# Optimization experiments

Measured on AMD Instinct MI355X. Metric: run time of the kernel, lower is better.

## Reference

```python
import jax, jax.numpy as jnp
import numpy as np

B, H, W, C = 4, 64, 64, 256
DQK = C // 16  # query/key channels = 16


def setup_inputs() -> dict:
    key = jax.random.key(0)
    ks = jax.random.split(key, 8)
    s = 0.05
    return {
        "x": jax.random.normal(ks[0], (B, H, W, C), dtype=jnp.float32),
        "wq": jax.random.normal(ks[1], (C, DQK), dtype=jnp.float32) * s,
        "bq": jax.random.normal(ks[2], (DQK,), dtype=jnp.float32) * s,
        "wk": jax.random.normal(ks[3], (C, DQK), dtype=jnp.float32) * s,
        "bk": jax.random.normal(ks[4], (DQK,), dtype=jnp.float32) * s,
        "wv": jax.random.normal(ks[5], (C, C), dtype=jnp.float32) * s,
        "bv": jax.random.normal(ks[6], (C,), dtype=jnp.float32) * s,
        "gamma": jax.random.normal(ks[7], (), dtype=jnp.float32),
    }


def reference(x, wq, bq, wk, bk, wv, bv, gamma):
    # 1x1 convs == per-pixel linear projections
    q = jnp.einsum('bhwc,cd->bhwd', x, wq) + bq          # [B,H,W,DQK]
    k = jnp.einsum('bhwc,cd->bhwd', x, wk) + bk          # [B,H,W,DQK]
    v = jnp.einsum('bhwc,cd->bhwd', x, wv) + bv          # [B,H,W,C]
    hw = H * W
    q = q.reshape(B, hw, DQK)
    k = k.reshape(B, hw, DQK)
    v = v.reshape(B, hw, C)
    energy = jnp.einsum('bnd,bmd->bnm', q, k)            # [B,HW,HW]
    attention = jax.nn.softmax(energy, axis=-1)
    out = jnp.einsum('bnm,bmc->bnc', attention, v)       # [B,HW,C]
    out = out.reshape(B, H, W, C)
    return out * gamma + x, attention
```

## Files before the change

### kernel.cpp

```cpp
#include <hip/hip_runtime.h>

typedef _Float16 half8 __attribute__((ext_vector_type(8)));
typedef _Float16 half4v __attribute__((ext_vector_type(4)));
typedef __fp16 fp16x2 __attribute__((ext_vector_type(2)));
typedef float f32x16 __attribute__((ext_vector_type(16)));
typedef float f32x4 __attribute__((ext_vector_type(4)));
typedef unsigned int uint2v __attribute__((ext_vector_type(2)));
typedef unsigned int uint4v __attribute__((ext_vector_type(4)));

#define MFMA16(a, b, c) __builtin_amdgcn_mfma_f32_32x32x16_f16((a), (b), (c), 0, 0, 0)
#define QSC 1.44269504088896f

#define OFF_WB   0
#define OFF_WQK  131072
#define OFF_QF   147456
#define OFF_KF   671744
#define OFF_VB   1196032
#define OFF_MLP  9584640

__device__ inline unsigned int pkf16(float a, float b) {
    union { fp16x2 h; unsigned int u; } cv;
    cv.h = __builtin_amdgcn_cvt_pkrtz(a, b);
    return cv.u;
}
__device__ inline half8 mk8(unsigned int w0, unsigned int w1, unsigned int w2, unsigned int w3) {
    union { unsigned int u[4]; half8 h; } cv;
    cv.u[0] = w0; cv.u[1] = w1; cv.u[2] = w2; cv.u[3] = w3; return cv.h;
}

__global__ __launch_bounds__(256) void k_prep(const float* __restrict__ wq,
                                              const float* __restrict__ wk,
                                              const float* __restrict__ wv,
                                              _Float16* __restrict__ WB,
                                              _Float16* __restrict__ WQK) {
    int idx = blockIdx.x * 256 + threadIdx.x;
    if (idx < 65536) {
        int j = idx & 7, l = (idx >> 3) & 63, kc = idx >> 12;
        int ct = (idx >> 9) & 7;
        int k = kc * 16 + (l >> 5) * 8 + j;
        int c = ct * 32 + (l & 31);
        WB[idx] = (_Float16)wv[k * 256 + c];
    } else if (idx < 65536 + 8192) {
        int t = idx - 65536;
        int j = t & 7, l = (t >> 3) & 63, kc = t >> 9;
        int k = kc * 16 + (l >> 5) * 8 + j;
        int c = l & 31;
        WQK[t] = (_Float16)((c < 16) ? wq[k * 16 + c] : wk[k * 16 + (c - 16)]);
    }
}

__global__ __launch_bounds__(256, 2) void k_proj(const float* __restrict__ x,
                                                 const float* __restrict__ bq,
                                                 const float* __restrict__ bk,
                                                 const float* __restrict__ bv,
                                                 const _Float16* __restrict__ WB,
                                                 const _Float16* __restrict__ WQK,
                                                 _Float16* __restrict__ Qf,
                                                 _Float16* __restrict__ Kf,
                                                 _Float16* __restrict__ VB) {
    const int tid = threadIdx.x;
    const int w = tid >> 6, l = tid & 63, lo = l & 31, h = l >> 5;
    const long rowbase = (long)blockIdx.x * 32;
    const float* xp = x + (rowbase + lo) * 256 + h * 8;

    f32x16 acc0 = {}, acc1 = {}, accQK = {};
#pragma unroll
    for (int kc = 0; kc < 16; ++kc) {
        float4 a0 = *(const float4*)(xp + kc * 16);
        float4 a1 = *(const float4*)(xp + kc * 16 + 4);
        half8 xf;
        xf[0] = (_Float16)a0.x; xf[1] = (_Float16)a0.y; xf[2] = (_Float16)a0.z; xf[3] = (_Float16)a0.w;
        xf[4] = (_Float16)a1.x; xf[5] = (_Float16)a1.y; xf[6] = (_Float16)a1.z; xf[7] = (_Float16)a1.w;
        half8 b0 = *(const half8*)(WB + ((kc * 8 + 2 * w) * 64 + l) * 8);
        half8 b1 = *(const half8*)(WB + ((kc * 8 + 2 * w + 1) * 64 + l) * 8);
        acc0 = MFMA16(xf, b0, acc0);
        acc1 = MFMA16(xf, b1, acc1);
        if (w == 0) {
            half8 bqk = *(const half8*)(WQK + (kc * 64 + l) * 8);
            accQK = MFMA16(xf, bqk, accQK);
        }
    }

    const int b = (int)(rowbase >> 12);
    const int k16base = (int)((rowbase & 4095) >> 4);
#pragma unroll
    for (int cti = 0; cti < 2; ++cti) {
        int ct = 2 * w + cti;
        f32x16 acc = cti ? acc1 : acc0;
        float bias = bv[ct * 32 + lo];
#pragma unroll
        for (int g = 0; g < 4; ++g) {
            int K16 = k16base + (g >> 1);
            int lanep = (g & 1) * 32 + lo;
            _Float16* dst = VB + ((((long)b * 256 + K16) * 8 + ct) * 64 + lanep) * 8 + 4 * h;
            half4v pv;
            pv[0] = (_Float16)(acc[4 * g + 0] + bias);
            pv[1] = (_Float16)(acc[4 * g + 1] + bias);
            pv[2] = (_Float16)(acc[4 * g + 2] + bias);
            pv[3] = (_Float16)(acc[4 * g + 3] + bias);
            *(half4v*)dst = pv;
        }
    }
    if (w == 0) {
        float bias = (lo < 16) ? bq[lo] : bk[lo - 16];
#pragma unroll
        for (int r = 0; r < 16; ++r) {
            int kl = (r & 3) + 8 * (r >> 2) + 4 * h;
            long n = rowbase + kl;
            float v = accQK[r] + bias;
            if (lo < 16) Qf[n * 16 + lo] = (_Float16)(v * QSC);
            else         Kf[n * 16 + (lo - 16)] = (_Float16)v;
        }
    }
}

__global__ __launch_bounds__(256, 4) void k_ml(const _Float16* __restrict__ Qf,
                                               const _Float16* __restrict__ Kf,
                                               float2* __restrict__ MLp) {
    const int bid = blockIdx.x;
    const int kh = bid & 1;
    const int qi = bid >> 1;
    const int b = qi >> 7, qt = qi & 127;
    const int tid = threadIdx.x, w = tid >> 6, l = tid & 63, lo = l & 31, h = l >> 5;
    const int qbase = qt * 32;

    half8 qf = *(const half8*)(Qf + (((long)b * 4096 + qbase + lo) << 4) + h * 8);
    const _Float16* Kb = Kf + ((long)b * 4096 << 4);

    float m = -3e38f, lsum = 0.f;
    for (int i = 0; i < 16; ++i) {
        int t = kh * 64 + i * 4 + w;
        half8 kf = *(const half8*)(Kb + ((t * 32 + lo) << 4) + h * 8);
        f32x16 e = MFMA16(kf, qf, (f32x16){});
        float t0 = fmaxf(fmaxf(e[0], e[1]), fmaxf(e[2], e[3]));
        float t1 = fmaxf(fmaxf(e[4], e[5]), fmaxf(e[6], e[7]));
        float t2 = fmaxf(fmaxf(e[8], e[9]), fmaxf(e[10], e[11]));
        float t3 = fmaxf(fmaxf(e[12], e[13]), fmaxf(e[14], e[15]));
        float tmax = fmaxf(fmaxf(t0, t1), fmaxf(t2, t3));
        tmax = fmaxf(tmax, __shfl_xor(tmax, 32));
        if (tmax > m) { lsum *= exp2f(m - tmax); m = tmax; }
        float ss = 0.f;
#pragma unroll
        for (int r = 0; r < 16; ++r) ss += exp2f(e[r] - m);
        lsum += ss;
    }
    lsum += __shfl_xor(lsum, 32);

    __shared__ float sm[4][32];
    __shared__ float sl[4][32];
    if (l < 32) { sm[w][lo] = m; sl[w][lo] = lsum; }
    __syncthreads();
    if (tid < 32) {
        float M = fmaxf(fmaxf(sm[0][tid], sm[1][tid]), fmaxf(sm[2][tid], sm[3][tid]));
        float L = sl[0][tid] * exp2f(sm[0][tid] - M) + sl[1][tid] * exp2f(sm[1][tid] - M) +
                  sl[2][tid] * exp2f(sm[2][tid] - M) + sl[3][tid] * exp2f(sm[3][tid] - M);
        float2 v; v.x = M; v.y = L;
        MLp[(((long)b * 4096 + qbase + tid) << 1) + kh] = v;
    }
}

#define RS 260
__global__ __launch_bounds__(256, 4) void k_attn(const float* __restrict__ x,
                                                 const float* __restrict__ gptr,
                                                 const _Float16* __restrict__ Qf,
                                                 const _Float16* __restrict__ Kf,
                                                 const _Float16* __restrict__ VB,
                                                 const float2* __restrict__ MLp,
                                                 float* __restrict__ out0,
                                                 float* __restrict__ attn) {
    const int bid = blockIdx.x;
    const int xcd = bid & 7, slot = bid >> 3;
    const int b = xcd >> 1;
    const int qt = (xcd & 1) * 64 + (slot & 63);
    const int sp = slot >> 6;
    const int tid = threadIdx.x, w = tid >> 6, l = tid & 63, lo = l & 31, h = l >> 5;
    const int qbase = qt * 32;

    half8 qf = *(const half8*)(Qf + (((long)b * 4096 + qbase + lo) << 4) + h * 8);
    const _Float16* Kb = Kf + ((long)b * 4096 << 4);

    const float2* mlrow = MLp + ((long)(b * 4096 + qbase + lo) << 1);
    float2 mla = mlrow[0];
    float2 mlc = mlrow[1];
    float Mrow = fmaxf(mla.x, mlc.x);
    const float S_lane = Mrow + __log2f(mla.y * exp2f(mla.x - Mrow) + mlc.y * exp2f(mlc.x - Mrow));

    const _Float16* vb = VB + (long)b * 256 * 8 * 64 * 8;

    __shared__ unsigned int pc[32 * RS];

    const int srow = tid >> 3;
    const int st7 = tid & 7;
    float* aout = attn + (long)b * 4096 * 4096 + ((long)(qbase + srow) << 12);

    f32x16 oacc[4] = {};

    for (int i = 0; i < 32; ++i) {
        int t = i * 4 + w;
        half8 kf = *(const half8*)(Kb + ((t * 32 + lo) << 4) + h * 8);
        f32x16 e = MFMA16(kf, qf, (f32x16){});
        float p[16];
#pragma unroll
        for (int r = 0; r < 16; ++r) p[r] = exp2f(e[r] - S_lane);

        unsigned int u0 = pkf16(p[0], p[1]),   x0 = pkf16(p[4], p[5]);
        unsigned int v0 = pkf16(p[2], p[3]),   y0 = pkf16(p[6], p[7]);
        unsigned int u1 = pkf16(p[8], p[9]),   x1 = pkf16(p[12], p[13]);
        unsigned int v1 = pkf16(p[10], p[11]), y1 = pkf16(p[14], p[15]);
        uint2v t0 = __builtin_amdgcn_permlane32_swap(u0, x0, false, false);
        uint2v t1 = __builtin_amdgcn_permlane32_swap(v0, y0, false, false);
        uint2v t2 = __builtin_amdgcn_permlane32_swap(u1, x1, false, false);
        uint2v t3 = __builtin_amdgcn_permlane32_swap(v1, y1, false, false);
        half8 pa0 = mk8(t0.x, t1.x, t0.y, t1.y);
        half8 pa1 = mk8(t2.x, t3.x, t2.y, t3.y);

        if ((i >> 4) == sp) {
            int base = lo * RS + ((i & 3) << 6) + (w << 4) + (h << 2);
            *(uint4v*)&pc[base]     = (uint4v){t0.x, t1.x, t0.y, t1.y};
            *(uint4v*)&pc[base + 8] = (uint4v){t2.x, t3.x, t2.y, t3.y};
            if ((i & 3) == 3) {
                __syncthreads();
                float* ap = aout + (i - 3) * 128 + st7 * 4;
                const unsigned int* src = &pc[srow * RS + st7 * 2];
#pragma unroll
                for (int seg = 0; seg < 16; ++seg) {
                    uint2v u = *(const uint2v*)(src + seg * 16);
                    union { unsigned int u; fp16x2 h; } a, c;
                    a.u = u.x; c.u = u.y;
                    f32x4 ov = { (float)a.h[0], (float)a.h[1], (float)c.h[0], (float)c.h[1] };
                    *(f32x4*)(ap + seg * 32) = ov;
                }
                __syncthreads();
            }
        }

#pragma unroll
        for (int ct = 0; ct < 4; ++ct) {
            int ctg = 4 * sp + ct;
            half8 vf0 = *(const half8*)(vb + (((long)(2 * t + 0) * 8 + ctg) * 64 + l) * 8);
            half8 vf1 = *(const half8*)(vb + (((long)(2 * t + 1) * 8 + ctg) * 64 + l) * 8);
            oacc[ct] = MFMA16(pa0, vf0, oacc[ct]);
            oacc[ct] = MFMA16(pa1, vf1, oacc[ct]);
        }
    }

    float* fO = (float*)pc;
#pragma unroll 1
    for (int ww = 0; ww < 4; ++ww) {
        __syncthreads();
        if (w == ww) {
#pragma unroll
            for (int ct = 0; ct < 4; ++ct) {
#pragma unroll
                for (int r = 0; r < 16; ++r) {
                    int row = (r & 3) + 8 * (r >> 2) + 4 * h;
                    float val = oacc[ct][r];
                    if (ww == 0) fO[row * 132 + ct * 32 + lo] = val;
                    else         fO[row * 132 + ct * 32 + lo] += val;
                }
            }
        }
    }
    __syncthreads();

    float gamma = *gptr;
    int cb = st7 << 4;
    long base = ((long)b * 4096 + qbase + srow) * 256 + sp * 128 + cb;
    const float* xp = x + base;
    float* op = out0 + base;
#pragma unroll
    for (int c0 = 0; c0 < 16; c0 += 4) {
        float4 xv = *(const float4*)(xp + c0);
        f32x4 ov;
        ov.x = gamma * fO[srow * 132 + cb + c0 + 0] + xv.x;
        ov.y = gamma * fO[srow * 132 + cb + c0 + 1] + xv.y;
        ov.z = gamma * fO[srow * 132 + cb + c0 + 2] + xv.z;
        ov.w = gamma * fO[srow * 132 + cb + c0 + 3] + xv.w;
        *(f32x4*)(op + c0) = ov;
    }
}

extern "C" void kernel_launch(void* const* d_in, const int* in_sizes, int n_in,
                              void* d_out, int out_size, void* d_ws, size_t ws_size,
                              hipStream_t stream) {
    const float* x  = (const float*)d_in[0];
    const float* wq = (const float*)d_in[1];
    const float* bq = (const float*)d_in[2];
    const float* wk = (const float*)d_in[3];
    const float* bk = (const float*)d_in[4];
    const float* wv = (const float*)d_in[5];
    const float* bv = (const float*)d_in[6];
    const float* gamma = (const float*)d_in[7];

    char* ws = (char*)d_ws;
    _Float16* WB  = (_Float16*)(ws + OFF_WB);
    _Float16* WQK = (_Float16*)(ws + OFF_WQK);
    _Float16* Qf  = (_Float16*)(ws + OFF_QF);
    _Float16* Kf  = (_Float16*)(ws + OFF_KF);
    _Float16* VB  = (_Float16*)(ws + OFF_VB);
    float2*   MLp = (float2*)(ws + OFF_MLP);

    float* out0 = (float*)d_out;
    float* attn = (float*)d_out + 4194304;

    k_prep<<<288, 256, 0, stream>>>(wq, wk, wv, WB, WQK);
    k_proj<<<512, 256, 0, stream>>>(x, bq, bk, bv, WB, WQK, Qf, Kf, VB);
    k_ml  <<<1024, 256, 0, stream>>>(Qf, Kf, MLp);
    k_attn<<<1024, 256, 0, stream>>>(x, gamma, Qf, Kf, VB, MLp, out0, attn);
}
```

Before: 152.4 us.

## Warp-specialize attention kernel: compute waves produce, store waves write attention map

Doubles the block to 512 threads. Four waves compute QK, exp and PV MFMAs, and four extra waves stream the fp16 probability tiles from a double-buffered shared staging area out to the fp32 attention matrix. The loop order is changed so each compute group of four tiles stashes its own half before the other, letting the stores of group g-1 overlap with the compute of group g. The cost is twice the shared memory, extra idle waves, and higher register pressure from launch_bounds(512,4), which may lower occupancy.

```diff
diff --git a/kernel.cpp b/kernel.cpp
--- a/kernel.cpp
+++ b/kernel.cpp
@@ -159,8 +159,8 @@
     }
 }
 
-#define RS 260
-__global__ __launch_bounds__(256, 4) void k_attn(const float* __restrict__ x,
+#define RSg 260
+__global__ __launch_bounds__(512, 4) void k_attn(const float* __restrict__ x,
                                                  const float* __restrict__ gptr,
                                                  const _Float16* __restrict__ Qf,
                                                  const _Float16* __restrict__ Kf,
@@ -173,82 +173,111 @@
     const int b = xcd >> 1;
     const int qt = (xcd & 1) * 64 + (slot & 63);
     const int sp = slot >> 6;
-    const int tid = threadIdx.x, w = tid >> 6, l = tid & 63, lo = l & 31, h = l >> 5;
+    const int tid = threadIdx.x;
+    const int wv8 = tid >> 6;
+    const bool isComp = wv8 < 4;
+    const int w = wv8 & 3;
+    const int l = tid & 63, lo = l & 31, h = l >> 5;
     const int qbase = qt * 32;
 
-    half8 qf = *(const half8*)(Qf + (((long)b * 4096 + qbase + lo) << 4) + h * 8);
+    __shared__ unsigned int pc[2][32 * RSg];
+
     const _Float16* Kb = Kf + ((long)b * 4096 << 4);
-
-    const float2* mlrow = MLp + ((long)(b * 4096 + qbase + lo) << 1);
-    float2 mla = mlrow[0];
-    float2 mlc = mlrow[1];
-    float Mrow = fmaxf(mla.x, mlc.x);
-    const float S_lane = Mrow + __log2f(mla.y * exp2f(mla.x - Mrow) + mlc.y * exp2f(mlc.x - Mrow));
-
     const _Float16* vb = VB + (long)b * 256 * 8 * 64 * 8;
 
-    __shared__ unsigned int pc[32 * RS];
-
-    const int srow = tid >> 3;
-    const int st7 = tid & 7;
-    float* aout = attn + (long)b * 4096 * 4096 + ((long)(qbase + srow) << 12);
+    half8 qf = {};
+    float S_lane = 0.f;
+    if (isComp) {
+        qf = *(const half8*)(Qf + (((long)b * 4096 + qbase + lo) << 4) + h * 8);
+        const float2* mlrow = MLp + ((long)(b * 4096 + qbase + lo) << 1);
+        float2 mla = mlrow[0];
+        float2 mlc = mlrow[1];
+        float Mrow = fmaxf(mla.x, mlc.x);
+        S_lane = Mrow + __log2f(mla.y * exp2f(mla.x - Mrow) + mlc.y * exp2f(mlc.x - Mrow));
+    }
+
+    const int stid = tid & 255;
+    const int srow = stid >> 3, st7 = stid & 7;
+    float* aoutrow = attn + (long)b * 4096 * 4096 + ((long)(qbase + srow) << 12) + sp * 2048;
 
     f32x16 oacc[4] = {};
 
-    for (int i = 0; i < 32; ++i) {
-        int t = i * 4 + w;
-        half8 kf = *(const half8*)(Kb + ((t * 32 + lo) << 4) + h * 8);
-        f32x16 e = MFMA16(kf, qf, (f32x16){});
-        float p[16];
-#pragma unroll
-        for (int r = 0; r < 16; ++r) p[r] = exp2f(e[r] - S_lane);
-
-        unsigned int u0 = pkf16(p[0], p[1]),   x0 = pkf16(p[4], p[5]);
-        unsigned int v0 = pkf16(p[2], p[3]),   y0 = pkf16(p[6], p[7]);
-        unsigned int u1 = pkf16(p[8], p[9]),   x1 = pkf16(p[12], p[13]);
-        unsigned int v1 = pkf16(p[10], p[11]), y1 = pkf16(p[14], p[15]);
-        uint2v t0 = __builtin_amdgcn_permlane32_swap(u0, x0, false, false);
-        uint2v t1 = __builtin_amdgcn_permlane32_swap(v0, y0, false, false);
-        uint2v t2 = __builtin_amdgcn_permlane32_swap(u1, x1, false, false);
-        uint2v t3 = __builtin_amdgcn_permlane32_swap(v1, y1, false, false);
-        half8 pa0 = mk8(t0.x, t1.x, t0.y, t1.y);
-        half8 pa1 = mk8(t2.x, t3.x, t2.y, t3.y);
-
-        if ((i >> 4) == sp) {
-            int base = lo * RS + ((i & 3) << 6) + (w << 4) + (h << 2);
-            *(uint4v*)&pc[base]     = (uint4v){t0.x, t1.x, t0.y, t1.y};
-            *(uint4v*)&pc[base + 8] = (uint4v){t2.x, t3.x, t2.y, t3.y};
-            if ((i & 3) == 3) {
-                __syncthreads();
-                float* ap = aout + (i - 3) * 128 + st7 * 4;
-                const unsigned int* src = &pc[srow * RS + st7 * 2];
-#pragma unroll
-                for (int seg = 0; seg < 16; ++seg) {
-                    uint2v u = *(const uint2v*)(src + seg * 16);
-                    union { unsigned int u; fp16x2 h; } a, c;
-                    a.u = u.x; c.u = u.y;
-                    f32x4 ov = { (float)a.h[0], (float)a.h[1], (float)c.h[0], (float)c.h[1] };
-                    *(f32x4*)(ap + seg * 32) = ov;
+#pragma unroll 1
+    for (int g = 0; g < 4; ++g) {
+        if (isComp) {
+#pragma unroll
+            for (int li = 0; li < 4; ++li) {
+#pragma unroll
+                for (int which = 0; which < 2; ++which) {
+                    const bool stash = (which == 0);
+                    const int i = (stash ? sp : (1 - sp)) * 16 + g * 4 + li;
+                    const int t = i * 4 + w;
+                    half8 kf = *(const half8*)(Kb + ((t * 32 + lo) << 4) + h * 8);
+                    f32x16 e = MFMA16(kf, qf, (f32x16){});
+                    float p[16];
+#pragma unroll
+                    for (int r = 0; r < 16; ++r) p[r] = exp2f(e[r] - S_lane);
+
+                    unsigned int u0 = pkf16(p[0], p[1]),   x0 = pkf16(p[4], p[5]);
+                    unsigned int v0 = pkf16(p[2], p[3]),   y0 = pkf16(p[6], p[7]);
+                    unsigned int u1 = pkf16(p[8], p[9]),   x1 = pkf16(p[12], p[13]);
+                    unsigned int v1 = pkf16(p[10], p[11]), y1 = pkf16(p[14], p[15]);
+                    uint2v t0 = __builtin_amdgcn_permlane32_swap(u0, x0, false, false);
+                    uint2v t1 = __builtin_amdgcn_permlane32_swap(v0, y0, false, false);
+                    uint2v t2 = __builtin_amdgcn_permlane32_swap(u1, x1, false, false);
+                    uint2v t3 = __builtin_amdgcn_permlane32_swap(v1, y1, false, false);
+                    half8 pa0 = mk8(t0.x, t1.x, t0.y, t1.y);
+                    half8 pa1 = mk8(t2.x, t3.x, t2.y, t3.y);
+
+                    if (stash) {
+                        int base = lo * RSg + (li << 6) + (w << 4) + (h << 2);
+                        *(uint4v*)&pc[g & 1][base]     = (uint4v){t0.x, t1.x, t0.y, t1.y};
+                        *(uint4v*)&pc[g & 1][base + 8] = (uint4v){t2.x, t3.x, t2.y, t3.y};
+                    }
+
+#pragma unroll
+                    for (int ct = 0; ct < 4; ++ct) {
+                        int ctg = 4 * sp + ct;
+                        half8 vf0 = *(const half8*)(vb + (((long)(2 * t + 0) * 8 + ctg) * 64 + l) * 8);
+                        half8 vf1 = *(const half8*)(vb + (((long)(2 * t + 1) * 8 + ctg) * 64 + l) * 8);
+                        oacc[ct] = MFMA16(pa0, vf0, oacc[ct]);
+                        oacc[ct] = MFMA16(pa1, vf1, oacc[ct]);
+                    }
                 }
-                __syncthreads();
             }
-        }
-
-#pragma unroll
-        for (int ct = 0; ct < 4; ++ct) {
-            int ctg = 4 * sp + ct;
-            half8 vf0 = *(const half8*)(vb + (((long)(2 * t + 0) * 8 + ctg) * 64 + l) * 8);
-            half8 vf1 = *(const half8*)(vb + (((long)(2 * t + 1) * 8 + ctg) * 64 + l) * 8);
-            oacc[ct] = MFMA16(pa0, vf0, oacc[ct]);
-            oacc[ct] = MFMA16(pa1, vf1, oacc[ct]);
-        }
-    }
-
-    float* fO = (float*)pc;
+        } else if (g > 0) {
+            const unsigned int* src = &pc[(g - 1) & 1][srow * RSg + st7 * 2];
+            float* ap = aoutrow + (g - 1) * 512 + st7 * 4;
+#pragma unroll
+            for (int seg = 0; seg < 16; ++seg) {
+                uint2v u = *(const uint2v*)(src + seg * 16);
+                union { unsigned int u; fp16x2 h; } ua, uc;
+                ua.u = u.x; uc.u = u.y;
+                f32x4 ov = { (float)ua.h[0], (float)ua.h[1], (float)uc.h[0], (float)uc.h[1] };
+                *(f32x4*)(ap + seg * 32) = ov;
+            }
+        }
+        __syncthreads();
+    }
+
+    if (!isComp) {
+        const unsigned int* src = &pc[1][srow * RSg + st7 * 2];
+        float* ap = aoutrow + 3 * 512 + st7 * 4;
+#pragma unroll
+        for (int seg = 0; seg < 16; ++seg) {
+            uint2v u = *(const uint2v*)(src + seg * 16);
+            union { unsigned int u; fp16x2 h; } ua, uc;
+            ua.u = u.x; uc.u = u.y;
+            f32x4 ov = { (float)ua.h[0], (float)ua.h[1], (float)uc.h[0], (float)uc.h[1] };
+            *(f32x4*)(ap + seg * 32) = ov;
+        }
+    }
+
+    float* fO = (float*)&pc[0][0];
 #pragma unroll 1
     for (int ww = 0; ww < 4; ++ww) {
         __syncthreads();
-        if (w == ww) {
+        if (isComp && w == ww) {
 #pragma unroll
             for (int ct = 0; ct < 4; ++ct) {
 #pragma unroll
@@ -263,20 +292,22 @@
     }
     __syncthreads();
 
-    float gamma = *gptr;
-    int cb = st7 << 4;
-    long base = ((long)b * 4096 + qbase + srow) * 256 + sp * 128 + cb;
-    const float* xp = x + base;
-    float* op = out0 + base;
-#pragma unroll
-    for (int c0 = 0; c0 < 16; c0 += 4) {
-        float4 xv = *(const float4*)(xp + c0);
-        f32x4 ov;
-        ov.x = gamma * fO[srow * 132 + cb + c0 + 0] + xv.x;
-        ov.y = gamma * fO[srow * 132 + cb + c0 + 1] + xv.y;
-        ov.z = gamma * fO[srow * 132 + cb + c0 + 2] + xv.z;
-        ov.w = gamma * fO[srow * 132 + cb + c0 + 3] + xv.w;
-        *(f32x4*)(op + c0) = ov;
+    if (!isComp) {
+        float gamma = *gptr;
+        int cb = st7 << 4;
+        long base = ((long)b * 4096 + qbase + srow) * 256 + sp * 128 + cb;
+        const float* xp = x + base;
+        float* op = out0 + base;
+#pragma unroll
+        for (int c0 = 0; c0 < 16; c0 += 4) {
+            float4 xv = *(const float4*)(xp + c0);
+            f32x4 ov;
+            ov.x = gamma * fO[srow * 132 + cb + c0 + 0] + xv.x;
+            ov.y = gamma * fO[srow * 132 + cb + c0 + 1] + xv.y;
+            ov.z = gamma * fO[srow * 132 + cb + c0 + 2] + xv.z;
+            ov.w = gamma * fO[srow * 132 + cb + c0 + 3] + xv.w;
+            *(f32x4*)(op + c0) = ov;
+        }
     }
 }
 
@@ -306,5 +337,5 @@
     k_prep<<<288, 256, 0, stream>>>(wq, wk, wv, WB, WQK);
     k_proj<<<512, 256, 0, stream>>>(x, bq, bk, bv, WB, WQK, Qf, Kf, VB);
     k_ml  <<<1024, 256, 0, stream>>>(Qf, Kf, MLp);
-    k_attn<<<1024, 256, 0, stream>>>(x, gamma, Qf, Kf, VB, MLp, out0, attn);
-}
+    k_attn<<<1024, 512, 0, stream>>>(x, gamma, Qf, Kf, VB, MLp, out0, attn);
+}
```

New measurement: 224.1 us. 47.0% more time.

## Stage fp16 attention probabilities in workspace and expand to fp32 in separate kernel

Applied to the files above, without the earlier changes.

The attention kernel no longer writes the fp32 attention matrix directly. It now stores fp16 probability tiles into a workspace buffer with simple contiguous stores. A new k_expand kernel then reads that buffer and writes the fp32 attention rows in full-row coalesced order. The aim is to take the large strided fp32 stores off the compute-heavy kernel, at the cost of an extra launch and an extra write plus read of about 128MB of fp16 data.

```diff
diff --git a/kernel.cpp b/kernel.cpp
--- a/kernel.cpp
+++ b/kernel.cpp
@@ -17,6 +17,7 @@
 #define OFF_KF   671744
 #define OFF_VB   1196032
 #define OFF_MLP  9584640
+#define OFF_PF   16777216
 
 __device__ inline unsigned int pkf16(float a, float b) {
     union { fp16x2 h; unsigned int u; } cv;
@@ -159,7 +160,7 @@
     }
 }
 
-#define RS 260
+#define RSg 260
 __global__ __launch_bounds__(256, 4) void k_attn(const float* __restrict__ x,
                                                  const float* __restrict__ gptr,
                                                  const _Float16* __restrict__ Qf,
@@ -167,7 +168,7 @@
                                                  const _Float16* __restrict__ VB,
                                                  const float2* __restrict__ MLp,
                                                  float* __restrict__ out0,
-                                                 float* __restrict__ attn) {
+                                                 unsigned int* __restrict__ Pf) {
     const int bid = blockIdx.x;
     const int xcd = bid & 7, slot = bid >> 3;
     const int b = xcd >> 1;
@@ -187,11 +188,9 @@
 
     const _Float16* vb = VB + (long)b * 256 * 8 * 64 * 8;
 
-    __shared__ unsigned int pc[32 * RS];
-
-    const int srow = tid >> 3;
-    const int st7 = tid & 7;
-    float* aout = attn + (long)b * 4096 * 4096 + ((long)(qbase + srow) << 12);
+    __shared__ unsigned int pc[32 * RSg];
+
+    unsigned int* PfT = Pf + (long)(b * 128 + qt) * 8 * 8192;
 
     f32x16 oacc[4] = {};
 
@@ -215,20 +214,18 @@
         half8 pa1 = mk8(t2.x, t3.x, t2.y, t3.y);
 
         if ((i >> 4) == sp) {
-            int base = lo * RS + ((i & 3) << 6) + (w << 4) + (h << 2);
+            int li = i & 3;
+            int base = lo * RSg + (li << 6) + (w << 4) + (h << 2);
             *(uint4v*)&pc[base]     = (uint4v){t0.x, t1.x, t0.y, t1.y};
             *(uint4v*)&pc[base + 8] = (uint4v){t2.x, t3.x, t2.y, t3.y};
-            if ((i & 3) == 3) {
+            if (li == 3) {
                 __syncthreads();
-                float* ap = aout + (i - 3) * 128 + st7 * 4;
-                const unsigned int* src = &pc[srow * RS + st7 * 2];
-#pragma unroll
-                for (int seg = 0; seg < 16; ++seg) {
-                    uint2v u = *(const uint2v*)(src + seg * 16);
-                    union { unsigned int u; fp16x2 h; } a, c;
-                    a.u = u.x; c.u = u.y;
-                    f32x4 ov = { (float)a.h[0], (float)a.h[1], (float)c.h[0], (float)c.h[1] };
-                    *(f32x4*)(ap + seg * 32) = ov;
+                int G = sp * 4 + ((i >> 2) & 3);
+                unsigned int* dst = PfT + (long)G * 8192;
+#pragma unroll
+                for (int it = 0; it < 8; ++it) {
+                    uint4v v = *(const uint4v*)&pc[(it * 4 + w) * RSg + l * 4];
+                    *(uint4v*)(dst + it * 1024 + w * 256 + l * 4) = v;
                 }
                 __syncthreads();
             }
@@ -264,6 +261,7 @@
     __syncthreads();
 
     float gamma = *gptr;
+    const int srow = tid >> 3, st7 = tid & 7;
     int cb = st7 << 4;
     long base = ((long)b * 4096 + qbase + srow) * 256 + sp * 128 + cb;
     const float* xp = x + base;
@@ -277,6 +275,33 @@
         ov.z = gamma * fO[srow * 132 + cb + c0 + 2] + xv.z;
         ov.w = gamma * fO[srow * 132 + cb + c0 + 3] + xv.w;
         *(f32x4*)(op + c0) = ov;
+    }
+}
+
+__global__ __launch_bounds__(256) void k_expand(const unsigned int* __restrict__ Pf,
+                                                float* __restrict__ attn) {
+    const int bid = blockIdx.x;
+    const int b = bid >> 8, qt = (bid >> 1) & 127, half = bid & 1;
+    const int tid = threadIdx.x, w = tid >> 6, l = tid & 63;
+    const unsigned int* PfT = Pf + (long)(b * 128 + qt) * 8 * 8192;
+    float* abase = attn + (long)b * 4096 * 4096 + (long)(qt * 32) * 4096;
+
+#pragma unroll 1
+    for (int rr = 0; rr < 4; ++rr) {
+        int r = half * 16 + w * 4 + rr;
+        float* arow = abase + (long)r * 4096;
+        const unsigned int* prow = PfT + r * 256;
+#pragma unroll
+        for (int j = 0; j < 16; ++j) {
+            int k = j * 256 + l * 4;
+            int G = k >> 9;
+            int offw = ((k & 511) >> 1);
+            uint2v u = *(const uint2v*)(prow + (long)G * 8192 + offw);
+            union { unsigned int u; fp16x2 h; } ua, uc;
+            ua.u = u.x; uc.u = u.y;
+            f32x4 ov = { (float)ua.h[0], (float)ua.h[1], (float)uc.h[0], (float)uc.h[1] };
+            *(f32x4*)(arow + k) = ov;
+        }
     }
 }
 
@@ -299,12 +324,14 @@
     _Float16* Kf  = (_Float16*)(ws + OFF_KF);
     _Float16* VB  = (_Float16*)(ws + OFF_VB);
     float2*   MLp = (float2*)(ws + OFF_MLP);
+    unsigned int* Pf = (unsigned int*)(ws + OFF_PF);
 
     float* out0 = (float*)d_out;
     float* attn = (float*)d_out + 4194304;
 
-    k_prep<<<288, 256, 0, stream>>>(wq, wk, wv, WB, WQK);
-    k_proj<<<512, 256, 0, stream>>>(x, bq, bk, bv, WB, WQK, Qf, Kf, VB);
-    k_ml  <<<1024, 256, 0, stream>>>(Qf, Kf, MLp);
-    k_attn<<<1024, 256, 0, stream>>>(x, gamma, Qf, Kf, VB, MLp, out0, attn);
-}
+    k_prep  <<<288, 256, 0, stream>>>(wq, wk, wv, WB, WQK);
+    k_proj  <<<512, 256, 0, stream>>>(x, bq, bk, bv, WB, WQK, Qf, Kf, VB);
+    k_ml    <<<1024, 256, 0, stream>>>(Qf, Kf, MLp);
+    k_attn  <<<1024, 256, 0, stream>>>(x, gamma, Qf, Kf, VB, MLp, out0, Pf);
+    k_expand<<<1024, 256, 0, stream>>>(Pf, attn);
+}
```

After: 205.4 us. +34.8%, slower.
